# Kernel tuning notes

Hardware: AMD Instinct MI355X
Metric: run time of the kernel (lower is better)

## Reference

```python
import jax, jax.numpy as jnp
import numpy as np

I_T = 0.5       # IoU threshold self.I_t
GAMMA = 2.0     # focal loss gamma
EPS = 1e-7      # focal loss eps clamp
BS, P, C_IN = 8, 2048, 512


def pairwise_iou(b):
    # b: (bs, P, 4) xyxy -> (bs, P, P), same math as torchvision box_iou (no +1)
    area = (b[..., 2] - b[..., 0]) * (b[..., 3] - b[..., 1])
    lt = jnp.maximum(b[:, :, None, :2], b[:, None, :, :2])
    rb = jnp.minimum(b[:, :, None, 2:], b[:, None, :, 2:])
    wh = jnp.clip(rb - lt, 0.0, None)
    inter = wh[..., 0] * wh[..., 1]
    return inter / (area[:, :, None] + area[:, None, :] - inter)


def assign_labels_weights(pre_score, labels, rois):
    # Vectorized, order-faithful version of the per-batch/per-class python loop.
    # Selected seeds per class c: proposals with pre_score[...,c] > 0.5 if more than
    # one, else the single argmax proposal (torch code falls back when k<=1).
    # Sequential `_I > old` running max over (c, j) in ascending order is equivalent
    # to a global first-occurrence argmax (strict >), so per-class max + running
    # compare with earlier-class tie preference reproduces it exactly.
    bs, Pn = pre_score.shape[0], pre_score.shape[1]
    iou = pairwise_iou(rois)                      # (bs, P, P)
    run_I = jnp.full((bs, Pn), -1.0, pre_score.dtype)
    run_w = jnp.ones((bs, Pn), pre_score.dtype)
    hits = []
    for c in range(3):
        s = pre_score[:, :, c]                    # (bs, P)
        th = s > 0.5
        cnt = th.sum(-1)
        onehot = jnp.arange(Pn)[None, :] == jnp.argmax(s, -1)[:, None]
        sel = jnp.where((cnt > 1)[:, None], th, onehot)
        sel = sel & (labels[:, c] != 0)[:, None]  # skip classes absent from image
        masked = jnp.where(sel[:, None, :], iou, -2.0)  # (bs, P, P)
        val = masked.max(-1)                      # best IoU vs any seed of class c
        jidx = masked.argmax(-1)
        cand_x = jnp.take_along_axis(s, jidx, axis=1)
        better = val > run_I
        run_w = jnp.where(better, cand_x, run_w)
        run_I = jnp.where(better, val, run_I)
        hits.append(val > I_T)
    hit = jnp.stack(hits, -1)                     # (bs, P, 3)
    bg = (~hit.any(-1))[..., None]
    y = jnp.concatenate([hit.astype(pre_score.dtype), bg.astype(pre_score.dtype)], -1)
    return y, run_w


def icr_forward(inputs, fc_w, fc_b, pre_score, labels, rois, num):
    bs = inputs.shape[0] // num
    xr = inputs @ fc_w + fc_b                     # (bs*P, 4)
    logit = jax.nn.softmax(xr.reshape(bs, num, 4), -1)
    ps = jax.lax.stop_gradient(pre_score)         # .clone().detach()
    lb = jax.lax.stop_gradient(labels)
    y, w = assign_labels_weights(ps, lb, rois)
    y = y.reshape(bs * num, 4)
    w = w.reshape(bs * num, 1)
    # FocalLoss(gamma=2, mode='none')
    p = jnp.clip(jax.nn.softmax(xr, -1), EPS, 1.0 - EPS)
    fl = -y * jnp.log(p) * (1.0 - p) ** GAMMA
    imbalance = y.sum(0)                          # (4,)
    loss = (w * fl / (imbalance + 1e-7)).reshape(bs, num, 4)
    lab = lb.at[:, 3].set(1.0)[:, None, :]        # lab[:,0,3]=1
    w_ = 10.0 * jnp.exp(logit) * (1.0 - lab) + lab
    loss = (loss * w_).sum() / bs
    return logit, loss


def setup_inputs():
    key = jax.random.key(0)
    k = jax.random.split(key, 6)
    inputs = jax.random.normal(k[0], (BS * P, C_IN), jnp.float32)
    fc_w = jax.random.normal(k[1], (C_IN, 4), jnp.float32) * 0.02
    fc_b = jnp.zeros((4,), jnp.float32)
    pre_score = jax.random.uniform(k[2], (BS, P, 4), dtype=jnp.float32)
    labels = (jax.random.uniform(k[3], (BS, 4)) < 0.5).astype(jnp.float32)
    labels = labels.at[:, 3].set(0.0)
    xy = jax.random.uniform(k[4], (BS, P, 2), dtype=jnp.float32) * 448.0
    wh = jax.random.uniform(k[5], (BS, P, 2), dtype=jnp.float32) * 63.0 + 1.0
    rois = jnp.concatenate([xy, xy + wh], -1)     # valid xyxy boxes in 512x512
    return {"inputs": inputs, "fc_w": fc_w, "fc_b": fc_b, "pre_score": pre_score,
            "labels": labels, "rois": rois, "num": P}


def reference(inputs, fc_w, fc_b, pre_score, labels, rois, num):
    return icr_forward(inputs, fc_w, fc_b, pre_score, labels, rois, num)
```

## Files before the change

kernel.cpp:

```cpp
#include <hip/hip_runtime.h>

typedef unsigned int u32;

#define BSZ 8
#define PN  2048
#define CIN 512
#define CAP 2056
#define NW  16


__global__ __launch_bounds__(256) void k_fc_softmax(
    const float* __restrict__ inp, const float* __restrict__ fcw,
    const float* __restrict__ fcb, float* __restrict__ logit)
{
  const int gw   = (blockIdx.x * blockDim.x + threadIdx.x) >> 6;
  const int lane = threadIdx.x & 63;
  const int kb   = lane << 2;

  const float4 wa0 = *(const float4*)(fcw + (kb + 0) * 4);
  const float4 wa1 = *(const float4*)(fcw + (kb + 1) * 4);
  const float4 wa2 = *(const float4*)(fcw + (kb + 2) * 4);
  const float4 wa3 = *(const float4*)(fcw + (kb + 3) * 4);
  const float4 wb0 = *(const float4*)(fcw + (256 + kb + 0) * 4);
  const float4 wb1 = *(const float4*)(fcw + (256 + kb + 1) * 4);
  const float4 wb2 = *(const float4*)(fcw + (256 + kb + 2) * 4);
  const float4 wb3 = *(const float4*)(fcw + (256 + kb + 3) * 4);
  const float4 bias = *(const float4*)fcb;

  #pragma unroll
  for (int rr = 0; rr < 4; ++rr) {
    const int r = (gw << 2) + rr;
    const float* row = inp + r * CIN;
    const float4 xa = *(const float4*)(row + kb);
    const float4 xb = *(const float4*)(row + 256 + kb);
    float a0 = xa.x*wa0.x + xa.y*wa1.x + xa.z*wa2.x + xa.w*wa3.x
             + xb.x*wb0.x + xb.y*wb1.x + xb.z*wb2.x + xb.w*wb3.x;
    float a1 = xa.x*wa0.y + xa.y*wa1.y + xa.z*wa2.y + xa.w*wa3.y
             + xb.x*wb0.y + xb.y*wb1.y + xb.z*wb2.y + xb.w*wb3.y;
    float a2 = xa.x*wa0.z + xa.y*wa1.z + xa.z*wa2.z + xa.w*wa3.z
             + xb.x*wb0.z + xb.y*wb1.z + xb.z*wb2.z + xb.w*wb3.z;
    float a3 = xa.x*wa0.w + xa.y*wa1.w + xa.z*wa2.w + xa.w*wa3.w
             + xb.x*wb0.w + xb.y*wb1.w + xb.z*wb2.w + xb.w*wb3.w;
    #pragma unroll
    for (int off = 32; off; off >>= 1) {
      a0 += __shfl_xor(a0, off);
      a1 += __shfl_xor(a1, off);
      a2 += __shfl_xor(a2, off);
      a3 += __shfl_xor(a3, off);
    }
    if (lane == 0) {
      a0 += bias.x; a1 += bias.y; a2 += bias.z; a3 += bias.w;
      const float m  = fmaxf(fmaxf(a0, a1), fmaxf(a2, a3));
      const float e0 = expf(a0 - m), e1 = expf(a1 - m);
      const float e2 = expf(a2 - m), e3 = expf(a3 - m);
      const float inv = 1.0f / (e0 + e1 + e2 + e3);
      float4 o; o.x = e0 * inv; o.y = e1 * inv; o.z = e2 * inv; o.w = e3 * inv;
      *(float4*)(logit + r * 4) = o;
    }
  }
}

__global__ __launch_bounds__(256) void k_select(
    const float* __restrict__ ps, const float* __restrict__ labels,
    const float* __restrict__ rois,
    int* __restrict__ meta, float* __restrict__ sList,
    float4* __restrict__ roiList)
{
  const int b = blockIdx.x / 3;
  const int c = blockIdx.x % 3;
  const int t = threadIdx.x;
  const int j0 = t * 8;

  float sv[8];
  int   flg = 0, cnt = 0;
  float vmax = -1e30f;
  int   jmax = 0;
  #pragma unroll
  for (int m = 0; m < 8; ++m) {
    const float s = ps[(b * PN + j0 + m) * 4 + c];
    sv[m] = s;
    if (s > 0.5f) { flg |= 1 << m; ++cnt; }
    if (s > vmax) { vmax = s; jmax = j0 + m; }
  }

  __shared__ float lv[256];
  __shared__ int   lj[256];
  __shared__ int   pre[256];
  lv[t] = vmax; lj[t] = jmax; pre[t] = cnt;
  __syncthreads();
  for (int off = 128; off > 0; off >>= 1) {
    if (t < off) {
      const float v2 = lv[t + off]; const int j2 = lj[t + off];
      if (v2 > lv[t] || (v2 == lv[t] && j2 < lj[t])) { lv[t] = v2; lj[t] = j2; }
    }
    __syncthreads();
  }
  for (int off = 1; off < 256; off <<= 1) {
    const int add = (t >= off) ? pre[t - off] : 0;
    __syncthreads();
    pre[t] += add;
    __syncthreads();
  }
  const int  totalTh = pre[255];
  const int  excl    = pre[t] - cnt;
  const int  jArg    = lj[0];
  const bool lab     = labels[b * 4 + c] != 0.0f;

  const int L    = (!lab) ? 0 : ((totalTh > 1) ? totalTh : 1);
  const int Lpad = (L + 7) & ~7;

  __shared__ float4 lastRoi;
  __shared__ float  lastS;
  float4* dstR = roiList + (b * 3 + c) * CAP;
  float*  dstS = sList   + (b * 3 + c) * CAP;
  const float4* rb = ((const float4*)rois) + b * PN;

  if (lab) {
    if (totalTh > 1) {
      int pos = excl;
      #pragma unroll
      for (int m = 0; m < 8; ++m) {
        if (flg & (1 << m)) {
          const float4 r = rb[j0 + m];
          dstR[pos] = r; dstS[pos] = sv[m];
          if (pos == L - 1) { lastRoi = r; lastS = sv[m]; }
          ++pos;
        }
      }
    } else if (t == (jArg >> 3)) {
      const float4 r = rb[jArg];
      dstR[0] = r; dstS[0] = sv[jArg & 7];
      lastRoi = r; lastS = sv[jArg & 7];
    }
  }
  __syncthreads();
  if (t < Lpad - L) { dstR[L + t] = lastRoi; dstS[L + t] = lastS; }
  if (t == 0) meta[b * 3 + c] = Lpad;
}

__global__ __launch_bounds__(1024) void k_assign(
    const float* __restrict__ rois, const float* __restrict__ labels,
    const int* __restrict__ meta, const float* __restrict__ sList,
    const float4* __restrict__ roiList, const float* __restrict__ logit,
    float* __restrict__ accum)
{
  const int b     = blockIdx.x >> 5;
  const int itile = blockIdx.x & 31;
  const int t     = threadIdx.x;
  const int lane  = t & 63;
  const int wv    = t >> 6;
  const int i     = (itile << 6) + lane;

  const float4 ri   = ((const float4*)rois)[b * PN + i];
  const float areai = (ri.z - ri.x) * (ri.w - ri.y);

  __shared__ float mn[3][NW][64];
  __shared__ float md[3][NW][64];
  __shared__ int   mp[3][NW][64];

  float BN[3], BD[3];
  int   BP[3];

  #pragma unroll
  for (int c = 0; c < 3; ++c) {
    float bn = -2.0f, bd = 1.0f;
    int   bp = 0;
    const int L = meta[b * 3 + c];
    const float4* base = roiList + (b * 3 + c) * CAP;
    const int C  = (((L + 15) >> 4) + 7) & ~7;
    const int g0 = wv * C;
    int g1 = g0 + C; if (g1 > L) g1 = L;
    for (int g = g0; g < g1; g += 8) {
      float4 r[8];
      #pragma unroll
      for (int u = 0; u < 8; ++u) r[u] = base[g + u];
      #pragma unroll
      for (int u = 0; u < 8; ++u) {
        const float4 rj = r[u];
        const float lx = fmaxf(ri.x, rj.x);
        const float ly = fmaxf(ri.y, rj.y);
        const float rx = fminf(ri.z, rj.z);
        const float ry = fminf(ri.w, rj.w);
        const float ww = fmaxf(rx - lx, 0.0f);
        const float hh = fmaxf(ry - ly, 0.0f);
        const float inter = ww * hh;
        const float areaj = (rj.z - rj.x) * (rj.w - rj.y);
        const float uni   = areai + areaj - inter;
        if (inter * bd > bn * uni) { bn = inter; bd = uni; bp = g + u; }
      }
    }
    mn[c][wv][lane] = bn; md[c][wv][lane] = bd; mp[c][wv][lane] = bp;
    BN[c] = bn; BD[c] = bd; BP[c] = bp;
  }
  __syncthreads();

  if (wv == 0) {
    #pragma unroll
    for (int c = 0; c < 3; ++c) {
      float bn = BN[c], bd = BD[c]; int bp = BP[c];
      for (int w2 = 1; w2 < NW; ++w2) {
        const float n = mn[c][w2][lane], d = md[c][w2][lane];
        const int   p = mp[c][w2][lane];
        if (n * bd > bn * d) { bn = n; bd = d; bp = p; }
      }
      BN[c] = bn; BD[c] = bd; BP[c] = bp;
    }
    const float v0 = BN[0] / BD[0];
    const float v1 = BN[1] / BD[1];
    const float v2 = BN[2] / BD[2];
    const float c0 = sList[(b * 3 + 0) * CAP + BP[0]];
    const float c1 = sList[(b * 3 + 1) * CAP + BP[1]];
    const float c2 = sList[(b * 3 + 2) * CAP + BP[2]];
    float runI = -1.0f, runw = 1.0f;
    if (v0 > runI) { runw = c0; runI = v0; }
    if (v1 > runI) { runw = c1; runI = v1; }
    if (v2 > runI) { runw = c2; runI = v2; }
    const float y0 = (v0 > 0.5f) ? 1.0f : 0.0f;
    const float y1 = (v1 > 0.5f) ? 1.0f : 0.0f;
    const float y2 = (v2 > 0.5f) ? 1.0f : 0.0f;
    const float y3 = (y0 + y1 + y2 == 0.0f) ? 1.0f : 0.0f;

    const float4 lg = ((const float4*)logit)[b * PN + i];
    const float lb0 = labels[b * 4 + 0];
    const float lb1 = labels[b * 4 + 1];
    const float lb2 = labels[b * 4 + 2];

    auto term = [&](const float l, const float yv, const float labv) -> float {
      const float p  = fminf(fmaxf(l, 1e-7f), 1.0f - 1e-7f);
      const float om = 1.0f - p;
      const float fl = -yv * logf(p) * om * om;
      const float wl = 10.0f * expf(l) * (1.0f - labv) + labv;
      return runw * fl * wl;
    };
    float s0 = term(lg.x, y0, lb0);
    float s1 = term(lg.y, y1, lb1);
    float s2 = term(lg.z, y2, lb2);
    float s3 = term(lg.w, y3, 1.0f);
    float z0 = y0, z1 = y1, z2 = y2, z3 = y3;
    #pragma unroll
    for (int off = 32; off; off >>= 1) {
      s0 += __shfl_xor(s0, off); s1 += __shfl_xor(s1, off);
      s2 += __shfl_xor(s2, off); s3 += __shfl_xor(s3, off);
      z0 += __shfl_xor(z0, off); z1 += __shfl_xor(z1, off);
      z2 += __shfl_xor(z2, off); z3 += __shfl_xor(z3, off);
    }
    if (lane == 0) {
      atomicAdd(&accum[0], s0); atomicAdd(&accum[1], s1);
      atomicAdd(&accum[2], s2); atomicAdd(&accum[3], s3);
      atomicAdd(&accum[4], z0); atomicAdd(&accum[5], z1);
      atomicAdd(&accum[6], z2); atomicAdd(&accum[7], z3);
    }
  }
}

__global__ void k_final(const float* __restrict__ accum, float* __restrict__ loss)
{
  if (threadIdx.x == 0) {
    float L = 0.0f;
    #pragma unroll
    for (int c = 0; c < 4; ++c) L += accum[c] / (accum[4 + c] + 1e-7f);
    loss[0] = L * 0.125f;
  }
}

extern "C" void kernel_launch(void* const* d_in, const int* in_sizes, int n_in,
                              void* d_out, int out_size, void* d_ws, size_t ws_size,
                              hipStream_t stream)
{
  (void)in_sizes; (void)n_in; (void)out_size; (void)ws_size;
  const float* inp    = (const float*)d_in[0];
  const float* fcw    = (const float*)d_in[1];
  const float* fcb    = (const float*)d_in[2];
  const float* ps     = (const float*)d_in[3];
  const float* labels = (const float*)d_in[4];
  const float* rois   = (const float*)d_in[5];
  float* out = (float*)d_out;

  float*  accum   = (float*)d_ws;
  int*    meta    = (int*)((char*)d_ws + 32);
  float*  sList   = (float*)((char*)d_ws + 1024);
  float4* roiList = (float4*)((char*)d_ws + 198400);

  hipMemsetAsync(accum, 0, 8 * sizeof(float), stream);
  k_fc_softmax<<<1024, 256, 0, stream>>>(inp, fcw, fcb, out);
  k_select   <<<24,   256, 0, stream>>>(ps, labels, rois, meta, sList, roiList);
  k_assign   <<<256, 1024, 0, stream>>>(rois, labels, meta, sList, roiList, out, accum);
  k_final    <<<1,     64, 0, stream>>>(accum, out + BSZ * PN * 4);
}
```

Baseline: 139.6 us.

## Fuse fc and select kernels, stage seed boxes in LDS, split assign across halves

After: 117.6 us, median of 2. -15.8%, faster.

```diff
diff --git a/kernel.cpp b/kernel.cpp
--- a/kernel.cpp
+++ b/kernel.cpp
@@ -1,74 +1,70 @@
 #include <hip/hip_runtime.h>
-
-typedef unsigned int u32;
 
 #define BSZ 8
 #define PN  2048
 #define CIN 512
-#define CAP 2056
+#define CAP 2048
 #define NW  16
 
 
-__global__ __launch_bounds__(256) void k_fc_softmax(
+__global__ __launch_bounds__(256) void k_front(
     const float* __restrict__ inp, const float* __restrict__ fcw,
-    const float* __restrict__ fcb, float* __restrict__ logit)
-{
-  const int gw   = (blockIdx.x * blockDim.x + threadIdx.x) >> 6;
-  const int lane = threadIdx.x & 63;
-  const int kb   = lane << 2;
-
-  const float4 wa0 = *(const float4*)(fcw + (kb + 0) * 4);
-  const float4 wa1 = *(const float4*)(fcw + (kb + 1) * 4);
-  const float4 wa2 = *(const float4*)(fcw + (kb + 2) * 4);
-  const float4 wa3 = *(const float4*)(fcw + (kb + 3) * 4);
-  const float4 wb0 = *(const float4*)(fcw + (256 + kb + 0) * 4);
-  const float4 wb1 = *(const float4*)(fcw + (256 + kb + 1) * 4);
-  const float4 wb2 = *(const float4*)(fcw + (256 + kb + 2) * 4);
-  const float4 wb3 = *(const float4*)(fcw + (256 + kb + 3) * 4);
-  const float4 bias = *(const float4*)fcb;
-
-  #pragma unroll
-  for (int rr = 0; rr < 4; ++rr) {
-    const int r = (gw << 2) + rr;
-    const float* row = inp + r * CIN;
-    const float4 xa = *(const float4*)(row + kb);
-    const float4 xb = *(const float4*)(row + 256 + kb);
-    float a0 = xa.x*wa0.x + xa.y*wa1.x + xa.z*wa2.x + xa.w*wa3.x
-             + xb.x*wb0.x + xb.y*wb1.x + xb.z*wb2.x + xb.w*wb3.x;
-    float a1 = xa.x*wa0.y + xa.y*wa1.y + xa.z*wa2.y + xa.w*wa3.y
-             + xb.x*wb0.y + xb.y*wb1.y + xb.z*wb2.y + xb.w*wb3.y;
-    float a2 = xa.x*wa0.z + xa.y*wa1.z + xa.z*wa2.z + xa.w*wa3.z
-             + xb.x*wb0.z + xb.y*wb1.z + xb.z*wb2.z + xb.w*wb3.z;
-    float a3 = xa.x*wa0.w + xa.y*wa1.w + xa.z*wa2.w + xa.w*wa3.w
-             + xb.x*wb0.w + xb.y*wb1.w + xb.z*wb2.w + xb.w*wb3.w;
-    #pragma unroll
-    for (int off = 32; off; off >>= 1) {
-      a0 += __shfl_xor(a0, off);
-      a1 += __shfl_xor(a1, off);
-      a2 += __shfl_xor(a2, off);
-      a3 += __shfl_xor(a3, off);
-    }
-    if (lane == 0) {
-      a0 += bias.x; a1 += bias.y; a2 += bias.z; a3 += bias.w;
-      const float m  = fmaxf(fmaxf(a0, a1), fmaxf(a2, a3));
-      const float e0 = expf(a0 - m), e1 = expf(a1 - m);
-      const float e2 = expf(a2 - m), e3 = expf(a3 - m);
-      const float inv = 1.0f / (e0 + e1 + e2 + e3);
-      float4 o; o.x = e0 * inv; o.y = e1 * inv; o.z = e2 * inv; o.w = e3 * inv;
-      *(float4*)(logit + r * 4) = o;
-    }
-  }
-}
-
-__global__ __launch_bounds__(256) void k_select(
-    const float* __restrict__ ps, const float* __restrict__ labels,
-    const float* __restrict__ rois,
+    const float* __restrict__ fcb, const float* __restrict__ ps,
+    const float* __restrict__ labels, const float* __restrict__ rois,
+    float* __restrict__ logit, float* __restrict__ accum,
     int* __restrict__ meta, float* __restrict__ sList,
-    float4* __restrict__ roiList)
-{
-  const int b = blockIdx.x / 3;
-  const int c = blockIdx.x % 3;
+    float* __restrict__ areaL, float4* __restrict__ roiList)
+{
   const int t = threadIdx.x;
+  if (blockIdx.x < 1024) {
+    const int gw   = (blockIdx.x * 256 + t) >> 6;
+    const int lane = t & 63;
+    const int kb   = lane << 2;
+    const float4 wa0 = *(const float4*)(fcw + (kb + 0) * 4);
+    const float4 wa1 = *(const float4*)(fcw + (kb + 1) * 4);
+    const float4 wa2 = *(const float4*)(fcw + (kb + 2) * 4);
+    const float4 wa3 = *(const float4*)(fcw + (kb + 3) * 4);
+    const float4 wb0 = *(const float4*)(fcw + (256 + kb + 0) * 4);
+    const float4 wb1 = *(const float4*)(fcw + (256 + kb + 1) * 4);
+    const float4 wb2 = *(const float4*)(fcw + (256 + kb + 2) * 4);
+    const float4 wb3 = *(const float4*)(fcw + (256 + kb + 3) * 4);
+    const float4 bias = *(const float4*)fcb;
+    #pragma unroll
+    for (int rr = 0; rr < 4; ++rr) {
+      const int r = (gw << 2) + rr;
+      const float* row = inp + r * CIN;
+      const float4 xa = *(const float4*)(row + kb);
+      const float4 xb = *(const float4*)(row + 256 + kb);
+      float a0 = xa.x*wa0.x + xa.y*wa1.x + xa.z*wa2.x + xa.w*wa3.x
+               + xb.x*wb0.x + xb.y*wb1.x + xb.z*wb2.x + xb.w*wb3.x;
+      float a1 = xa.x*wa0.y + xa.y*wa1.y + xa.z*wa2.y + xa.w*wa3.y
+               + xb.x*wb0.y + xb.y*wb1.y + xb.z*wb2.y + xb.w*wb3.y;
+      float a2 = xa.x*wa0.z + xa.y*wa1.z + xa.z*wa2.z + xa.w*wa3.z
+               + xb.x*wb0.z + xb.y*wb1.z + xb.z*wb2.z + xb.w*wb3.z;
+      float a3 = xa.x*wa0.w + xa.y*wa1.w + xa.z*wa2.w + xa.w*wa3.w
+               + xb.x*wb0.w + xb.y*wb1.w + xb.z*wb2.w + xb.w*wb3.w;
+      #pragma unroll
+      for (int off = 32; off; off >>= 1) {
+        a0 += __shfl_xor(a0, off); a1 += __shfl_xor(a1, off);
+        a2 += __shfl_xor(a2, off); a3 += __shfl_xor(a3, off);
+      }
+      if (lane == 0) {
+        a0 += bias.x; a1 += bias.y; a2 += bias.z; a3 += bias.w;
+        const float m  = fmaxf(fmaxf(a0, a1), fmaxf(a2, a3));
+        const float e0 = expf(a0 - m), e1 = expf(a1 - m);
+        const float e2 = expf(a2 - m), e3 = expf(a3 - m);
+        const float inv = 1.0f / (e0 + e1 + e2 + e3);
+        float4 o; o.x = e0*inv; o.y = e1*inv; o.z = e2*inv; o.w = e3*inv;
+        *(float4*)(logit + r * 4) = o;
+      }
+    }
+    return;
+  }
+
+  const int bc = blockIdx.x - 1024;
+  if (bc == 0 && t < 8) accum[t] = 0.0f;
+  const int b = bc / 3;
+  const int c = bc % 3;
   const int j0 = t * 8;
 
   float sv[8];
@@ -105,14 +101,14 @@
   const int  excl    = pre[t] - cnt;
   const int  jArg    = lj[0];
   const bool lab     = labels[b * 4 + c] != 0.0f;
-
-  const int L    = (!lab) ? 0 : ((totalTh > 1) ? totalTh : 1);
-  const int Lpad = (L + 7) & ~7;
+  const int  L    = (!lab) ? 0 : ((totalTh > 1) ? totalTh : 1);
+  const int  Lpad = (L + 7) & ~7;
 
   __shared__ float4 lastRoi;
-  __shared__ float  lastS;
-  float4* dstR = roiList + (b * 3 + c) * CAP;
-  float*  dstS = sList   + (b * 3 + c) * CAP;
+  __shared__ float  lastS, lastA;
+  float4* dstR = roiList + bc * CAP;
+  float*  dstS = sList   + bc * CAP;
+  float*  dstA = areaL   + bc * CAP;
   const float4* rb = ((const float4*)rois) + b * PN;
 
   if (lab) {
@@ -122,134 +118,183 @@
       for (int m = 0; m < 8; ++m) {
         if (flg & (1 << m)) {
           const float4 r = rb[j0 + m];
-          dstR[pos] = r; dstS[pos] = sv[m];
-          if (pos == L - 1) { lastRoi = r; lastS = sv[m]; }
+          const float  a = (r.z - r.x) * (r.w - r.y);
+          dstR[pos] = r; dstS[pos] = sv[m]; dstA[pos] = a;
+          if (pos == L - 1) { lastRoi = r; lastS = sv[m]; lastA = a; }
           ++pos;
         }
       }
     } else if (t == (jArg >> 3)) {
       const float4 r = rb[jArg];
-      dstR[0] = r; dstS[0] = sv[jArg & 7];
-      lastRoi = r; lastS = sv[jArg & 7];
-    }
-  }
-  __syncthreads();
-  if (t < Lpad - L) { dstR[L + t] = lastRoi; dstS[L + t] = lastS; }
-  if (t == 0) meta[b * 3 + c] = Lpad;
-}
-
-__global__ __launch_bounds__(1024) void k_assign(
-    const float* __restrict__ rois, const float* __restrict__ labels,
-    const int* __restrict__ meta, const float* __restrict__ sList,
-    const float4* __restrict__ roiList, const float* __restrict__ logit,
-    float* __restrict__ accum)
-{
-  const int b     = blockIdx.x >> 5;
-  const int itile = blockIdx.x & 31;
+      const float  a = (r.z - r.x) * (r.w - r.y);
+      dstR[0] = r; dstS[0] = sv[jArg & 7]; dstA[0] = a;
+      lastRoi = r; lastS = sv[jArg & 7]; lastA = a;
+    }
+  }
+  __syncthreads();
+  if (t < Lpad - L) { dstR[L + t] = lastRoi; dstS[L + t] = lastS; dstA[L + t] = lastA; }
+  if (t == 0) meta[bc] = Lpad;
+}
+
+__global__ __launch_bounds__(1024, 8) void k_assign(
+    const float* __restrict__ rois, const int* __restrict__ meta,
+    const float4* __restrict__ roiList, const float* __restrict__ areaL,
+    float* __restrict__ pbn, float* __restrict__ pbd, int* __restrict__ pbp)
+{
+  const int blk   = blockIdx.x;
+  const int h     = blk & 1;
+  const int itile = (blk >> 1) & 31;
+  const int b     = blk >> 6;
   const int t     = threadIdx.x;
   const int lane  = t & 63;
   const int wv    = t >> 6;
-  const int i     = (itile << 6) + lane;
-
-  const float4 ri   = ((const float4*)rois)[b * PN + i];
+
+  __shared__ __align__(16) char ldsraw[61440];
+  float4* sroi  = (float4*)ldsraw;
+  float*  sarea = (float*)(ldsraw + 49152);
+  float*  mn    = (float*)ldsraw;
+  float*  md    = (float*)(ldsraw + 12288);
+  int*    mp    = (int*)(ldsraw + 24576);
+
+  int startc[3], cntc[3];
+  #pragma unroll
+  for (int c = 0; c < 3; ++c) {
+    const int L  = meta[b * 3 + c];
+    const int L2 = ((L >> 1) + 7) & ~7;
+    const int s0 = h ? L2 : 0;
+    const int e0 = h ? L  : L2;
+    startc[c] = s0;
+    cntc[c]   = e0 - s0;
+    if (t < cntc[c]) {
+      sroi [c * 1024 + t] = roiList[(b * 3 + c) * CAP + s0 + t];
+      sarea[c * 1024 + t] = areaL  [(b * 3 + c) * CAP + s0 + t];
+    }
+  }
+  const int i = (itile << 6) + lane;
+  const float4 ri = ((const float4*)rois)[b * PN + i];
   const float areai = (ri.z - ri.x) * (ri.w - ri.y);
-
-  __shared__ float mn[3][NW][64];
-  __shared__ float md[3][NW][64];
-  __shared__ int   mp[3][NW][64];
-
-  float BN[3], BD[3];
-  int   BP[3];
-
+  __syncthreads();
+
+  float BN[3], BD[3]; int BP[3];
   #pragma unroll
   for (int c = 0; c < 3; ++c) {
-    float bn = -2.0f, bd = 1.0f;
-    int   bp = 0;
-    const int L = meta[b * 3 + c];
-    const float4* base = roiList + (b * 3 + c) * CAP;
-    const int C  = (((L + 15) >> 4) + 7) & ~7;
-    const int g0 = wv * C;
-    int g1 = g0 + C; if (g1 > L) g1 = L;
-    for (int g = g0; g < g1; g += 8) {
-      float4 r[8];
-      #pragma unroll
-      for (int u = 0; u < 8; ++u) r[u] = base[g + u];
-      #pragma unroll
-      for (int u = 0; u < 8; ++u) {
-        const float4 rj = r[u];
-        const float lx = fmaxf(ri.x, rj.x);
-        const float ly = fmaxf(ri.y, rj.y);
-        const float rx = fminf(ri.z, rj.z);
-        const float ry = fminf(ri.w, rj.w);
-        const float ww = fmaxf(rx - lx, 0.0f);
-        const float hh = fmaxf(ry - ly, 0.0f);
-        const float inter = ww * hh;
-        const float areaj = (rj.z - rj.x) * (rj.w - rj.y);
-        const float uni   = areai + areaj - inter;
-        if (inter * bd > bn * uni) { bn = inter; bd = uni; bp = g + u; }
-      }
-    }
-    mn[c][wv][lane] = bn; md[c][wv][lane] = bd; mp[c][wv][lane] = bp;
-    BN[c] = bn; BD[c] = bd; BP[c] = bp;
-  }
-  __syncthreads();
-
+    const int cnt = cntc[c];
+    const int C   = (((cnt + 15) >> 4) + 7) & ~7;
+    const int g0  = wv * C;
+    int g1 = g0 + C; if (g1 > cnt) g1 = cnt;
+    float nA = -2.0f, dA = 1.0f, nB = -2.0f, dB = 1.0f;
+    int   pA = 0, pB = 0;
+    const float4* rbase = sroi  + c * 1024;
+    const float*  abase = sarea + c * 1024;
+
+    auto upd = [&](float& n, float& d, int& p,
+                   const float4 rj, const float aj, const int pos) {
+      const float lx = fmaxf(ri.x, rj.x), ly = fmaxf(ri.y, rj.y);
+      const float rx = fminf(ri.z, rj.z), ry = fminf(ri.w, rj.w);
+      const float ww = fmaxf(rx - lx, 0.0f), hh = fmaxf(ry - ly, 0.0f);
+      const float inter = ww * hh;
+      const float uni   = areai + aj - inter;
+      if (inter * d > n * uni) { n = inter; d = uni; p = pos; }
+    };
+
+    for (int g = g0; g < g1; g += 4) {
+      const float4 r0 = rbase[g], r1 = rbase[g+1], r2 = rbase[g+2], r3 = rbase[g+3];
+      const float  a0 = abase[g], a1 = abase[g+1], a2 = abase[g+2], a3 = abase[g+3];
+      upd(nA, dA, pA, r0, a0, g);
+      upd(nB, dB, pB, r2, a2, g + 2);
+      upd(nA, dA, pA, r1, a1, g + 1);
+      upd(nB, dB, pB, r3, a3, g + 3);
+    }
+    const float tB = nB * dA, tA = nA * dB;
+    if (tB > tA || (tB == tA && pB < pA)) { nA = nB; dA = dB; pA = pB; }
+    BN[c] = nA; BD[c] = dA; BP[c] = pA + startc[c];
+  }
+  __syncthreads();
+  #pragma unroll
+  for (int c = 0; c < 3; ++c) {
+    mn[(c * NW + wv) * 64 + lane] = BN[c];
+    md[(c * NW + wv) * 64 + lane] = BD[c];
+    mp[(c * NW + wv) * 64 + lane] = BP[c];
+  }
+  __syncthreads();
   if (wv == 0) {
     #pragma unroll
     for (int c = 0; c < 3; ++c) {
       float bn = BN[c], bd = BD[c]; int bp = BP[c];
       for (int w2 = 1; w2 < NW; ++w2) {
-        const float n = mn[c][w2][lane], d = md[c][w2][lane];
-        const int   p = mp[c][w2][lane];
+        const float n = mn[(c * NW + w2) * 64 + lane];
+        const float d = md[(c * NW + w2) * 64 + lane];
+        const int   p = mp[(c * NW + w2) * 64 + lane];
         if (n * bd > bn * d) { bn = n; bd = d; bp = p; }
       }
-      BN[c] = bn; BD[c] = bd; BP[c] = bp;
-    }
-    const float v0 = BN[0] / BD[0];
-    const float v1 = BN[1] / BD[1];
-    const float v2 = BN[2] / BD[2];
-    const float c0 = sList[(b * 3 + 0) * CAP + BP[0]];
-    const float c1 = sList[(b * 3 + 1) * CAP + BP[1]];
-    const float c2 = sList[(b * 3 + 2) * CAP + BP[2]];
-    float runI = -1.0f, runw = 1.0f;
-    if (v0 > runI) { runw = c0; runI = v0; }
-    if (v1 > runI) { runw = c1; runI = v1; }
-    if (v2 > runI) { runw = c2; runI = v2; }
-    const float y0 = (v0 > 0.5f) ? 1.0f : 0.0f;
-    const float y1 = (v1 > 0.5f) ? 1.0f : 0.0f;
-    const float y2 = (v2 > 0.5f) ? 1.0f : 0.0f;
-    const float y3 = (y0 + y1 + y2 == 0.0f) ? 1.0f : 0.0f;
-
-    const float4 lg = ((const float4*)logit)[b * PN + i];
-    const float lb0 = labels[b * 4 + 0];
-    const float lb1 = labels[b * 4 + 1];
-    const float lb2 = labels[b * 4 + 2];
-
-    auto term = [&](const float l, const float yv, const float labv) -> float {
-      const float p  = fminf(fmaxf(l, 1e-7f), 1.0f - 1e-7f);
-      const float om = 1.0f - p;
-      const float fl = -yv * logf(p) * om * om;
-      const float wl = 10.0f * expf(l) * (1.0f - labv) + labv;
-      return runw * fl * wl;
-    };
-    float s0 = term(lg.x, y0, lb0);
-    float s1 = term(lg.y, y1, lb1);
-    float s2 = term(lg.z, y2, lb2);
-    float s3 = term(lg.w, y3, 1.0f);
-    float z0 = y0, z1 = y1, z2 = y2, z3 = y3;
-    #pragma unroll
-    for (int off = 32; off; off >>= 1) {
-      s0 += __shfl_xor(s0, off); s1 += __shfl_xor(s1, off);
-      s2 += __shfl_xor(s2, off); s3 += __shfl_xor(s3, off);
-      z0 += __shfl_xor(z0, off); z1 += __shfl_xor(z1, off);
-      z2 += __shfl_xor(z2, off); z3 += __shfl_xor(z3, off);
-    }
-    if (lane == 0) {
-      atomicAdd(&accum[0], s0); atomicAdd(&accum[1], s1);
-      atomicAdd(&accum[2], s2); atomicAdd(&accum[3], s3);
-      atomicAdd(&accum[4], z0); atomicAdd(&accum[5], z1);
-      atomicAdd(&accum[6], z2); atomicAdd(&accum[7], z3);
-    }
+      const int o = ((b * 3 + c) * 2 + h) * PN + i;
+      pbn[o] = bn; pbd[o] = bd; pbp[o] = bp;
+    }
+  }
+}
+
+__global__ __launch_bounds__(256) void k_back(
+    const float* __restrict__ pbn, const float* __restrict__ pbd,
+    const int* __restrict__ pbp, const float* __restrict__ sList,
+    const float* __restrict__ logit, const float* __restrict__ labels,
+    float* __restrict__ accum)
+{
+  const int t  = threadIdx.x;
+  const int gi = blockIdx.x * 256 + t;
+  const int b  = gi >> 11;
+  const int i  = gi & (PN - 1);
+
+  float v[3], sc[3];
+  #pragma unroll
+  for (int c = 0; c < 3; ++c) {
+    const int o0 = ((b * 3 + c) * 2) * PN + i;
+    float n = pbn[o0], d = pbd[o0]; int p = pbp[o0];
+    const float n1 = pbn[o0 + PN], d1 = pbd[o0 + PN];
+    const int   p1 = pbp[o0 + PN];
+    if (n1 * d > n * d1) { n = n1; d = d1; p = p1; }
+    v[c]  = n / d;
+    sc[c] = sList[(b * 3 + c) * CAP + p];
+  }
+  float runI = -1.0f, runw = 1.0f;
+  if (v[0] > runI) { runw = sc[0]; runI = v[0]; }
+  if (v[1] > runI) { runw = sc[1]; runI = v[1]; }
+  if (v[2] > runI) { runw = sc[2]; runI = v[2]; }
+  const float y0 = (v[0] > 0.5f) ? 1.0f : 0.0f;
+  const float y1 = (v[1] > 0.5f) ? 1.0f : 0.0f;
+  const float y2 = (v[2] > 0.5f) ? 1.0f : 0.0f;
+  const float y3 = (y0 + y1 + y2 == 0.0f) ? 1.0f : 0.0f;
+
+  const float4 lg = ((const float4*)logit)[gi];
+  const float lb0 = labels[b * 4 + 0];
+  const float lb1 = labels[b * 4 + 1];
+  const float lb2 = labels[b * 4 + 2];
+
+  auto term = [&](const float l, const float yv, const float labv) -> float {
+    const float p  = fminf(fmaxf(l, 1e-7f), 1.0f - 1e-7f);
+    const float om = 1.0f - p;
+    const float fl = -yv * logf(p) * om * om;
+    const float wl = 10.0f * expf(l) * (1.0f - labv) + labv;
+    return runw * fl * wl;
+  };
+  float s[8];
+  s[0] = term(lg.x, y0, lb0); s[1] = term(lg.y, y1, lb1);
+  s[2] = term(lg.z, y2, lb2); s[3] = term(lg.w, y3, 1.0f);
+  s[4] = y0; s[5] = y1; s[6] = y2; s[7] = y3;
+
+  #pragma unroll
+  for (int k = 0; k < 8; ++k)
+    #pragma unroll
+    for (int off = 32; off; off >>= 1) s[k] += __shfl_xor(s[k], off);
+
+  __shared__ float red[4][8];
+  const int wv = t >> 6;
+  if ((t & 63) == 0)
+    #pragma unroll
+    for (int k = 0; k < 8; ++k) red[wv][k] = s[k];
+  __syncthreads();
+  if (t < 8) {
+    const float sum = red[0][t] + red[1][t] + red[2][t] + red[3][t];
+    atomicAdd(&accum[t], sum);
   }
 }
 
@@ -276,14 +321,19 @@
   const float* rois   = (const float*)d_in[5];
   float* out = (float*)d_out;
 
-  float*  accum   = (float*)d_ws;
-  int*    meta    = (int*)((char*)d_ws + 32);
-  float*  sList   = (float*)((char*)d_ws + 1024);
-  float4* roiList = (float4*)((char*)d_ws + 198400);
-
-  hipMemsetAsync(accum, 0, 8 * sizeof(float), stream);
-  k_fc_softmax<<<1024, 256, 0, stream>>>(inp, fcw, fcb, out);
-  k_select   <<<24,   256, 0, stream>>>(ps, labels, rois, meta, sList, roiList);
-  k_assign   <<<256, 1024, 0, stream>>>(rois, labels, meta, sList, roiList, out, accum);
-  k_final    <<<1,     64, 0, stream>>>(accum, out + BSZ * PN * 4);
-}
+  char* ws = (char*)d_ws;
+  float*  accum   = (float*) (ws);
+  int*    meta    = (int*)   (ws + 64);
+  float*  sList   = (float*) (ws + 1024);
+  float*  areaL   = (float*) (ws + 197632);
+  float4* roiL    = (float4*)(ws + 394240);
+  float*  pbn     = (float*) (ws + 1180672);
+  float*  pbd     = (float*) (ws + 1573888);
+  int*    pbp     = (int*)   (ws + 1967104);
+
+  k_front <<<1048, 256, 0, stream>>>(inp, fcw, fcb, ps, labels, rois,
+                                     out, accum, meta, sList, areaL, roiL);
+  k_assign<<<512, 1024, 0, stream>>>(rois, meta, roiL, areaL, pbn, pbd, pbp);
+  k_back  <<<64,   256, 0, stream>>>(pbn, pbd, pbp, sList, out, labels, accum);
+  k_final <<<1,     64, 0, stream>>>(accum, out + BSZ * PN * 4);
+}
```
